# Kernel optimization log

Hardware: AMD Instinct MI355X
Metric: run time of the kernel (lower is better)

## Reference

```python
import jax, jax.numpy as jnp
import numpy as np

N_NODES = 25000
N_EDGES = 100000
NODE_IN = 8
EDGE_IN = 4
HID = 32


def _glorot(key, shape):
    fan_in, fan_out = shape[0], shape[-1]
    s = jnp.sqrt(2.0 / (fan_in + fan_out))
    return jax.random.normal(key, shape, dtype=jnp.float32) * s


def setup_inputs() -> dict:
    key = jax.random.key(0)
    ks = jax.random.split(key, 16)
    x = jax.random.normal(ks[0], (N_NODES, NODE_IN), dtype=jnp.float32)
    edge_index = jax.random.randint(ks[1], (2, N_EDGES), 0, N_NODES, dtype=jnp.int64)
    edge_attr = jax.random.uniform(ks[2], (N_EDGES, EDGE_IN), dtype=jnp.float32)
    params = {
        # conv1: edge MLP (edge_in -> node_in*hid), root lin (node_in->hid, no bias), bias
        'w_mlp1': _glorot(ks[3], (EDGE_IN, NODE_IN * HID)),
        'b_mlp1': jnp.zeros((NODE_IN * HID,), jnp.float32),
        'root1': _glorot(ks[4], (NODE_IN, HID)),
        'bias1': jnp.zeros((HID,), jnp.float32),
        # conv2
        'w_mlp2': _glorot(ks[5], (EDGE_IN, HID * HID)),
        'b_mlp2': jnp.zeros((HID * HID,), jnp.float32),
        'root2': _glorot(ks[6], (HID, HID)),
        'bias2': jnp.zeros((HID,), jnp.float32),
        # conv3
        'w_mlp3': _glorot(ks[7], (EDGE_IN, HID * HID)),
        'b_mlp3': jnp.zeros((HID * HID,), jnp.float32),
        'root3': _glorot(ks[8], (HID, HID)),
        'bias3': jnp.zeros((HID,), jnp.float32),
        # output head: Linear(hid,hid) -> ReLU -> Linear(hid,1)
        'w_out1': _glorot(ks[9], (HID, HID)),
        'b_out1': jnp.zeros((HID,), jnp.float32),
        'w_out2': _glorot(ks[10], (HID, 1)),
        'b_out2': jnp.zeros((1,), jnp.float32),
    }
    return {'x': x, 'edge_index': edge_index, 'edge_attr': edge_attr, **params}


def _nnconv(x, src, dst, edge_attr, w_mlp, b_mlp, root, bias, in_dim, out_dim, num_nodes):
    # edge MLP -> per-edge weight matrix [E, in, out]
    w_e = jax.nn.relu(edge_attr @ w_mlp + b_mlp).reshape(-1, in_dim, out_dim)
    # gather source features, per-edge matvec
    msg = jnp.einsum('ei,eio->eo', x[src], w_e)  # [E, out]
    # scatter-mean into target nodes
    agg = jax.ops.segment_sum(msg, dst, num_segments=num_nodes)
    cnt = jax.ops.segment_sum(jnp.ones((msg.shape[0],), msg.dtype), dst, num_segments=num_nodes)
    agg = agg / jnp.maximum(cnt, 1.0)[:, None]
    return agg + x @ root + bias


def reference(x, edge_index, edge_attr,
              w_mlp1, b_mlp1, root1, bias1,
              w_mlp2, b_mlp2, root2, bias2,
              w_mlp3, b_mlp3, root3, bias3,
              w_out1, b_out1, w_out2, b_out2):
    src, dst = edge_index[0], edge_index[1]
    n = x.shape[0]
    h = jax.nn.relu(_nnconv(x, src, dst, edge_attr, w_mlp1, b_mlp1, root1, bias1, NODE_IN, HID, n))
    h = jax.nn.relu(_nnconv(h, src, dst, edge_attr, w_mlp2, b_mlp2, root2, bias2, HID, HID, n))
    h = jax.nn.relu(_nnconv(h, src, dst, edge_attr, w_mlp3, b_mlp3, root3, bias3, HID, HID, n))
    h = jax.nn.relu(h @ w_out1 + b_out1)
    return h @ w_out2 + b_out2  # [N, 1]
```

## Files before the change

kernel.cpp:

```cpp
#include <hip/hip_runtime.h>

#define HID 32

__global__ void count_kernel(const int* __restrict__ dst, float* __restrict__ cnt, int E) {
    int e = blockIdx.x * blockDim.x + threadIdx.x;
    if (e < E) atomicAdd(cnt + dst[e], 1.0f);
}

template<int IN>
__global__ __launch_bounds__(256) void edge_kernel(
    const float* __restrict__ h_in,
    const int* __restrict__ src, const int* __restrict__ dst,
    const float* __restrict__ ea,
    const float* __restrict__ w_mlp,
    const float* __restrict__ b_mlp,
    float* __restrict__ agg,
    int E)
{
    const int lane = threadIdx.x & 31;
    const int grp  = (blockIdx.x * blockDim.x + threadIdx.x) >> 5;
    const int ngrp = (gridDim.x * blockDim.x) >> 5;

    float w0[IN], w1[IN], w2[IN], w3[IN], br[IN];
    #pragma unroll
    for (int i = 0; i < IN; ++i) {
        int c = i * HID + lane;
        w0[i] = w_mlp[c];
        w1[i] = w_mlp[IN * HID + c];
        w2[i] = w_mlp[2 * IN * HID + c];
        w3[i] = w_mlp[3 * IN * HID + c];
        br[i] = b_mlp[c];
    }

    for (int e = grp; e < E; e += ngrp) {
        int s = src[e], d = dst[e];
        float4 a = *(const float4*)(ea + (size_t)e * 4);
        const float* xs = h_in + (size_t)s * IN;
        float acc = 0.f;
        #pragma unroll
        for (int i = 0; i < IN; ++i) {
            float t = fmaf(a.x, w0[i], br[i]);
            t = fmaf(a.y, w1[i], t);
            t = fmaf(a.z, w2[i], t);
            t = fmaf(a.w, w3[i], t);
            t = fmaxf(t, 0.f);
            acc = fmaf(xs[i], t, acc);
        }
        atomicAdd(agg + (size_t)d * HID + lane, acc);
    }
}

template<int IN>
__global__ __launch_bounds__(256) void node_kernel(
    const float* __restrict__ x_in,
    const float* __restrict__ agg,
    const float* __restrict__ cnt,
    const float* __restrict__ root,
    const float* __restrict__ bias,
    float* __restrict__ h_out,
    int N)
{
    int idx = blockIdx.x * blockDim.x + threadIdx.x;
    int v = idx >> 5, o = idx & 31;
    if (v >= N) return;
    float r = bias[o];
    const float* xv = x_in + (size_t)v * IN;
    #pragma unroll
    for (int i = 0; i < IN; ++i)
        r = fmaf(xv[i], root[i * HID + o], r);
    float m = agg[(size_t)v * HID + o] / fmaxf(cnt[v], 1.0f);
    h_out[(size_t)v * HID + o] = fmaxf(m + r, 0.f);
}

__global__ __launch_bounds__(256) void head_kernel(
    const float* __restrict__ h,
    const float* __restrict__ w1, const float* __restrict__ b1,
    const float* __restrict__ w2, const float* __restrict__ b2,
    float* __restrict__ out, int N)
{
    int idx = blockIdx.x * blockDim.x + threadIdx.x;
    int v = idx >> 5, o = idx & 31;
    if (v >= N) return;
    float t = b1[o];
    const float* hv = h + (size_t)v * HID;
    #pragma unroll
    for (int i = 0; i < HID; ++i)
        t = fmaf(hv[i], w1[i * HID + o], t);
    t = fmaxf(t, 0.f) * w2[o];
    #pragma unroll
    for (int d = 16; d > 0; d >>= 1)
        t += __shfl_down(t, d, 32);
    if (o == 0) out[v] = t + b2[0];
}

extern "C" void kernel_launch(void* const* d_in, const int* in_sizes, int n_in,
                              void* d_out, int out_size, void* d_ws, size_t ws_size,
                              hipStream_t stream)
{
    const float* x      = (const float*)d_in[0];
    const int*   ei     = (const int*)d_in[1];
    const float* ea     = (const float*)d_in[2];
    const float* w_mlp1 = (const float*)d_in[3];
    const float* b_mlp1 = (const float*)d_in[4];
    const float* root1  = (const float*)d_in[5];
    const float* bias1  = (const float*)d_in[6];
    const float* w_mlp2 = (const float*)d_in[7];
    const float* b_mlp2 = (const float*)d_in[8];
    const float* root2  = (const float*)d_in[9];
    const float* bias2  = (const float*)d_in[10];
    const float* w_mlp3 = (const float*)d_in[11];
    const float* b_mlp3 = (const float*)d_in[12];
    const float* root3  = (const float*)d_in[13];
    const float* bias3  = (const float*)d_in[14];
    const float* w_out1 = (const float*)d_in[15];
    const float* b_out1 = (const float*)d_in[16];
    const float* w_out2 = (const float*)d_in[17];
    const float* b_out2 = (const float*)d_in[18];

    const int NODE_IN = 8;
    const int N = in_sizes[0] / NODE_IN;
    const int E = in_sizes[2] / 4;
    const int* src = ei;
    const int* dst = ei + E;

    char* ws = (char*)d_ws;
    size_t off = 0;
    auto carve = [&](size_t bytes) {
        char* p = ws + off;
        off += (bytes + 255) & ~(size_t)255;
        return p;
    };
    float* cnt = (float*)carve((size_t)N * 4);
    float* agg = (float*)carve((size_t)N * HID * 4);
    float* h1  = (float*)carve((size_t)N * HID * 4);
    float* h2  = (float*)carve((size_t)N * HID * 4);
    float* outp = (float*)d_out;

    const int TB = 256;
    const int nodeBlocks = (N * HID + TB - 1) / TB;
    const int edgeBlocks = 1024;
    const int cntBlocks  = (E + TB - 1) / TB;

    hipMemsetAsync(cnt, 0, (size_t)N * 4, stream);
    hipMemsetAsync(agg, 0, (size_t)N * HID * 4, stream);
    count_kernel<<<cntBlocks, TB, 0, stream>>>(dst, cnt, E);

    edge_kernel<8><<<edgeBlocks, TB, 0, stream>>>(x, src, dst, ea, w_mlp1, b_mlp1, agg, E);
    node_kernel<8><<<nodeBlocks, TB, 0, stream>>>(x, agg, cnt, root1, bias1, h1, N);

    hipMemsetAsync(agg, 0, (size_t)N * HID * 4, stream);
    edge_kernel<32><<<edgeBlocks, TB, 0, stream>>>(h1, src, dst, ea, w_mlp2, b_mlp2, agg, E);
    node_kernel<32><<<nodeBlocks, TB, 0, stream>>>(h1, agg, cnt, root2, bias2, h2, N);

    hipMemsetAsync(agg, 0, (size_t)N * HID * 4, stream);
    edge_kernel<32><<<edgeBlocks, TB, 0, stream>>>(h2, src, dst, ea, w_mlp3, b_mlp3, agg, E);
    node_kernel<32><<<nodeBlocks, TB, 0, stream>>>(h2, agg, cnt, root3, bias3, h1, N);

    head_kernel<<<nodeBlocks, TB, 0, stream>>>(h1, w_out1, b_out1, w_out2, b_out2, outp, N);
}
```

Baseline: 216.1 us.

## Fuse count into edge pass, zero agg in node pass, fuse head, prefetch edges

Folds the degree count into the first edge kernel and clears agg inside the node kernel, which removes the separate count kernel and two memsets. The last node update is fused with the output head, and h is shared across lanes with shuffles. The edge loop software-prefetches the next edge's indices, attributes and source features as float4 vectors, and the edge grid is halved to 512 blocks. This trades several launches and memory passes for more registers per thread and fewer resident waves to hide atomic latency.

```diff
diff --git a/kernel.cpp b/kernel.cpp
--- a/kernel.cpp
+++ b/kernel.cpp
@@ -2,12 +2,7 @@
 
 #define HID 32
 
-__global__ void count_kernel(const int* __restrict__ dst, float* __restrict__ cnt, int E) {
-    int e = blockIdx.x * blockDim.x + threadIdx.x;
-    if (e < E) atomicAdd(cnt + dst[e], 1.0f);
-}
-
-template<int IN>
+template<int IN, bool DO_COUNT>
 __global__ __launch_bounds__(256) void edge_kernel(
     const float* __restrict__ h_in,
     const int* __restrict__ src, const int* __restrict__ dst,
@@ -15,6 +10,7 @@
     const float* __restrict__ w_mlp,
     const float* __restrict__ b_mlp,
     float* __restrict__ agg,
+    float* __restrict__ cnt,
     int E)
 {
     const int lane = threadIdx.x & 31;
@@ -32,28 +28,59 @@
         br[i] = b_mlp[c];
     }
 
-    for (int e = grp; e < E; e += ngrp) {
-        int s = src[e], d = dst[e];
-        float4 a = *(const float4*)(ea + (size_t)e * 4);
-        const float* xs = h_in + (size_t)s * IN;
+    int e = grp;
+    if (e >= E) return;
+    int s = src[e], d = dst[e];
+    float4 a = *(const float4*)(ea + (size_t)e * 4);
+    float4 xv[IN / 4];
+    #pragma unroll
+    for (int q = 0; q < IN / 4; ++q)
+        xv[q] = *(const float4*)(h_in + (size_t)s * IN + q * 4);
+
+    while (true) {
+        const int e2 = e + ngrp;
+        const bool more = (e2 < E);
+        int s2 = 0, d2 = 0;
+        float4 a2 = make_float4(0.f, 0.f, 0.f, 0.f);
+        float4 xv2[IN / 4];
+        if (more) {
+            s2 = src[e2]; d2 = dst[e2];
+            a2 = *(const float4*)(ea + (size_t)e2 * 4);
+            #pragma unroll
+            for (int q = 0; q < IN / 4; ++q)
+                xv2[q] = *(const float4*)(h_in + (size_t)s2 * IN + q * 4);
+        }
+
         float acc = 0.f;
         #pragma unroll
-        for (int i = 0; i < IN; ++i) {
-            float t = fmaf(a.x, w0[i], br[i]);
-            t = fmaf(a.y, w1[i], t);
-            t = fmaf(a.z, w2[i], t);
-            t = fmaf(a.w, w3[i], t);
-            t = fmaxf(t, 0.f);
-            acc = fmaf(xs[i], t, acc);
+        for (int q = 0; q < IN / 4; ++q) {
+            const float xs[4] = { xv[q].x, xv[q].y, xv[q].z, xv[q].w };
+            #pragma unroll
+            for (int j = 0; j < 4; ++j) {
+                const int i = q * 4 + j;
+                float t = fmaf(a.x, w0[i], br[i]);
+                t = fmaf(a.y, w1[i], t);
+                t = fmaf(a.z, w2[i], t);
+                t = fmaf(a.w, w3[i], t);
+                t = fmaxf(t, 0.f);
+                acc = fmaf(xs[j], t, acc);
+            }
         }
         atomicAdd(agg + (size_t)d * HID + lane, acc);
+        if (DO_COUNT && lane == 0) atomicAdd(cnt + d, 1.0f);
+
+        if (!more) break;
+        e = e2; s = s2; d = d2; a = a2;
+        #pragma unroll
+        for (int q = 0; q < IN / 4; ++q) xv[q] = xv2[q];
     }
+    (void)s;
 }
 
-template<int IN>
+template<int IN, bool ZERO_AGG>
 __global__ __launch_bounds__(256) void node_kernel(
     const float* __restrict__ x_in,
-    const float* __restrict__ agg,
+    float* __restrict__ agg,
     const float* __restrict__ cnt,
     const float* __restrict__ root,
     const float* __restrict__ bias,
@@ -69,11 +96,16 @@
     for (int i = 0; i < IN; ++i)
         r = fmaf(xv[i], root[i * HID + o], r);
     float m = agg[(size_t)v * HID + o] / fmaxf(cnt[v], 1.0f);
+    if (ZERO_AGG) agg[(size_t)v * HID + o] = 0.f;
     h_out[(size_t)v * HID + o] = fmaxf(m + r, 0.f);
 }
 
-__global__ __launch_bounds__(256) void head_kernel(
-    const float* __restrict__ h,
+__global__ __launch_bounds__(256) void node_head_kernel(
+    const float* __restrict__ x_in,
+    const float* __restrict__ agg,
+    const float* __restrict__ cnt,
+    const float* __restrict__ root,
+    const float* __restrict__ bias,
     const float* __restrict__ w1, const float* __restrict__ b1,
     const float* __restrict__ w2, const float* __restrict__ b2,
     float* __restrict__ out, int N)
@@ -81,15 +113,22 @@
     int idx = blockIdx.x * blockDim.x + threadIdx.x;
     int v = idx >> 5, o = idx & 31;
     if (v >= N) return;
-    float t = b1[o];
-    const float* hv = h + (size_t)v * HID;
+    float r = bias[o];
+    const float* xv = x_in + (size_t)v * HID;
     #pragma unroll
     for (int i = 0; i < HID; ++i)
-        t = fmaf(hv[i], w1[i * HID + o], t);
+        r = fmaf(xv[i], root[i * HID + o], r);
+    float m = agg[(size_t)v * HID + o] / fmaxf(cnt[v], 1.0f);
+    float h = fmaxf(m + r, 0.f);
+
+    float t = b1[o];
+    #pragma unroll
+    for (int i = 0; i < HID; ++i)
+        t = fmaf(__shfl(h, i, 32), w1[i * HID + o], t);
     t = fmaxf(t, 0.f) * w2[o];
     #pragma unroll
-    for (int d = 16; d > 0; d >>= 1)
-        t += __shfl_down(t, d, 32);
+    for (int dd = 16; dd > 0; dd >>= 1)
+        t += __shfl_down(t, dd, 32);
     if (o == 0) out[v] = t + b2[0];
 }
 
@@ -132,29 +171,24 @@
     };
     float* cnt = (float*)carve((size_t)N * 4);
     float* agg = (float*)carve((size_t)N * HID * 4);
+    size_t zero_bytes = (size_t)((char*)agg - (char*)cnt) + (size_t)N * HID * 4;
     float* h1  = (float*)carve((size_t)N * HID * 4);
     float* h2  = (float*)carve((size_t)N * HID * 4);
     float* outp = (float*)d_out;
 
     const int TB = 256;
     const int nodeBlocks = (N * HID + TB - 1) / TB;
-    const int edgeBlocks = 1024;
-    const int cntBlocks  = (E + TB - 1) / TB;
+    const int edgeBlocks = 512;
 
-    hipMemsetAsync(cnt, 0, (size_t)N * 4, stream);
-    hipMemsetAsync(agg, 0, (size_t)N * HID * 4, stream);
-    count_kernel<<<cntBlocks, TB, 0, stream>>>(dst, cnt, E);
+    hipMemsetAsync(cnt, 0, zero_bytes, stream);
 
-    edge_kernel<8><<<edgeBlocks, TB, 0, stream>>>(x, src, dst, ea, w_mlp1, b_mlp1, agg, E);
-    node_kernel<8><<<nodeBlocks, TB, 0, stream>>>(x, agg, cnt, root1, bias1, h1, N);
+    edge_kernel<8, true><<<edgeBlocks, TB, 0, stream>>>(x, src, dst, ea, w_mlp1, b_mlp1, agg, cnt, E);
+    node_kernel<8, true><<<nodeBlocks, TB, 0, stream>>>(x, agg, cnt, root1, bias1, h1, N);
 
-    hipMemsetAsync(agg, 0, (size_t)N * HID * 4, stream);
-    edge_kernel<32><<<edgeBlocks, TB, 0, stream>>>(h1, src, dst, ea, w_mlp2, b_mlp2, agg, E);
-    node_kernel<32><<<nodeBlocks, TB, 0, stream>>>(h1, agg, cnt, root2, bias2, h2, N);
+    edge_kernel<32, false><<<edgeBlocks, TB, 0, stream>>>(h1, src, dst, ea, w_mlp2, b_mlp2, agg, cnt, E);
+    node_kernel<32, true><<<nodeBlocks, TB, 0, stream>>>(h1, agg, cnt, root2, bias2, h2, N);
 
-    hipMemsetAsync(agg, 0, (size_t)N * HID * 4, stream);
-    edge_kernel<32><<<edgeBlocks, TB, 0, stream>>>(h2, src, dst, ea, w_mlp3, b_mlp3, agg, E);
-    node_kernel<32><<<nodeBlocks, TB, 0, stream>>>(h2, agg, cnt, root3, bias3, h1, N);
-
-    head_kernel<<<nodeBlocks, TB, 0, stream>>>(h1, w_out1, b_out1, w_out2, b_out2, outp, N);
+    edge_kernel<32, false><<<edgeBlocks, TB, 0, stream>>>(h2, src, dst, ea, w_mlp3, b_mlp3, agg, cnt, E);
+    node_head_kernel<<<nodeBlocks, TB, 0, stream>>>(h2, agg, cnt, root3, bias3,
+                                                    w_out1, b_out1, w_out2, b_out2, outp, N);
 }
```

Result: faster. 210.4 us (-2.7%).
